# Kernel tuning notes

Hardware: AMD Instinct MI355X
Metric: run time of the kernel (lower is better)

Reference implementation:

```python
import jax, jax.numpy as jnp
import numpy as np

B, T, D = 2, 2048, 512
H, W = 8, 32
d = D // H


def setup_inputs() -> dict:
    key = jax.random.key(0)
    ks = jax.random.split(key, 9)
    s = 1.0 / np.sqrt(D)
    return {
        "x": jax.random.normal(ks[0], (B, T, D), dtype=jnp.float32),
        "wq": jax.random.normal(ks[1], (D, D), dtype=jnp.float32) * s,
        "bq": jnp.zeros((D,), dtype=jnp.float32),
        "wk": jax.random.normal(ks[2], (D, D), dtype=jnp.float32) * s,
        "bk": jnp.zeros((D,), dtype=jnp.float32),
        "wv": jax.random.normal(ks[3], (D, D), dtype=jnp.float32) * s,
        "bv": jnp.zeros((D,), dtype=jnp.float32),
        "wo": jax.random.normal(ks[4], (D, D), dtype=jnp.float32) * s,
        "bo": jnp.zeros((D,), dtype=jnp.float32),
    }


def _local_attn(x, wq, bq, wk, bk, wv, bv, wo, bo):
    Bx, Tx, Dx = x.shape
    # projections (weights stored as [D_in, D_out])
    Q = (x @ wq + bq).reshape(Bx, Tx, H, d).transpose(0, 2, 1, 3)  # [B,H,T,d]
    K = (x @ wk + bk).reshape(Bx, Tx, H, d).transpose(0, 2, 1, 3)
    V = (x @ wv + bv).reshape(Bx, Tx, H, d).transpose(0, 2, 1, 3)
    # zero-pad time axis by W on both sides (matches F.pad value=0; NO masking,
    # padded zero keys get score 0 and participate in softmax like the original)
    Kp = jnp.pad(K, ((0, 0), (0, 0), (W, W), (0, 0)))  # [B,H,T+2W,d]
    Vp = jnp.pad(V, ((0, 0), (0, 0), (W, W), (0, 0)))
    idx = jnp.arange(Tx)[:, None] + jnp.arange(2 * W + 1)[None, :]  # [T, 2W+1]
    K_loc = Kp[:, :, idx, :]  # [B,H,T,2W+1,d]
    V_loc = Vp[:, :, idx, :]
    scores = jnp.einsum("bhtd,bhtwd->bhtw", Q, K_loc) / jnp.sqrt(jnp.asarray(d, x.dtype))
    attn = jax.nn.softmax(scores, axis=-1)
    out = jnp.einsum("bhtw,bhtwd->bhtd", attn, V_loc)  # [B,H,T,d]
    out = out.transpose(0, 2, 1, 3).reshape(Bx, Tx, Dx)
    return out @ wo + bo


def reference(x, wq, bq, wk, bk, wv, bv, wo, bo):
    return _local_attn(x, wq, bq, wk, bk, wv, bv, wo, bo)
```

## Files before the change

kernel.cpp:

```cpp
#include <hip/hip_runtime.h>

using f16x8 = __attribute__((ext_vector_type(8))) _Float16;
using f16x4 = __attribute__((ext_vector_type(4))) _Float16;
using f32x4 = __attribute__((ext_vector_type(4))) float;

#define T_SEQ 2048
#define D_MODEL 512
#define NH 8
#define HD 64
#define NB 2
#define M_ROWS (NB * T_SEQ)

#define GLOAD_LDS16(g, l)                                              \
  __builtin_amdgcn_global_load_lds(                                    \
      (const __attribute__((address_space(1))) void*)(g),              \
      (__attribute__((address_space(3))) void*)(l), 16, 0, 0)

__global__ __launch_bounds__(256) void cvt_all(
    const float* __restrict__ x, const float* __restrict__ wq,
    const float* __restrict__ wk, const float* __restrict__ wv,
    const float* __restrict__ wo, const float* __restrict__ bq,
    const float* __restrict__ bk, const float* __restrict__ bv,
    _Float16* __restrict__ xh, _Float16* __restrict__ wT,
    float* __restrict__ bias3) {
  int bid = blockIdx.x;
  int i = threadIdx.x;
  if (bid < 2048) {
    int idx = (bid * 256 + i) * 4;
    float4 v = *(const float4*)(x + idx);
    f16x4 h;
    h[0] = (_Float16)v.x; h[1] = (_Float16)v.y;
    h[2] = (_Float16)v.z; h[3] = (_Float16)v.w;
    *(f16x4*)(xh + idx) = h;
    return;
  }
  bid -= 2048;
  const int z = bid >> 8;
  const int by = (bid >> 4) & 15;
  const int bx = bid & 15;
  const float* w = z == 0 ? wq : z == 1 ? wk : z == 2 ? wv : wo;
  __shared__ float t[32][33];
  int r0 = by * 32, c0 = bx * 32;
#pragma unroll
  for (int p = 0; p < 4; ++p) {
    int e = p * 256 + i;
    int row = e >> 5, col = e & 31;
    t[row][col] = w[(size_t)(r0 + row) * D_MODEL + c0 + col];
  }
  __syncthreads();
  _Float16* o = wT + (size_t)z * D_MODEL * D_MODEL;
#pragma unroll
  for (int p = 0; p < 4; ++p) {
    int e = p * 256 + i;
    int orow = e >> 5, ocol = e & 31;
    o[(size_t)(c0 + orow) * D_MODEL + r0 + ocol] = (_Float16)t[ocol][orow];
  }
  if (bx == 0 && by == 0 && z < 3) {
    const float* bb = z == 0 ? bq : z == 1 ? bk : bv;
#pragma unroll
    for (int p = 0; p < 2; ++p)
      bias3[z * D_MODEL + p * 256 + i] = bb[p * 256 + i];
  }
}

template <int OUT_F32, int BM>
__global__ __launch_bounds__(256) void gemm_bt(
    const _Float16* __restrict__ A, const _Float16* __restrict__ BtBase,
    const float* __restrict__ biasBase, void* outBase) {
  constexpr int BN = 128;
  constexpr int WROWS = (BM >= 128) ? 2 : 1;
  constexpr int WCOLS = 4 / WROWS;
  constexpr int MF = BM / WROWS / 16;
  constexpr int NF = BN / WCOLS / 16;
  constexpr int NT = D_MODEL / 32;
  const int z = blockIdx.z;
  const _Float16* Bt = BtBase + (size_t)z * D_MODEL * D_MODEL;
  const float* bias = biasBase + z * D_MODEL;
  const int m0 = blockIdx.y * BM;
  const int n0 = blockIdx.x * BN;
  __shared__ _Float16 At[2][BM * 32];
  __shared__ _Float16 Bts[2][BN * 32];
  const int tid = threadIdx.x;
  const int l = tid & 63;
  const int wv = tid >> 6;
  const int wm = wv / WCOLS, wn = wv % WCOLS;
  const int r16 = l & 15, g4 = l >> 4;
  f32x4 acc[MF][NF] = {};

  auto stage = [&](int bb, int k0) {
#pragma unroll
    for (int cc = 0; cc < BM / 64; ++cc) {
      int c = tid + cc * 256;
      int row = c >> 2, part = c & 3;
      GLOAD_LDS16(&A[(size_t)(m0 + row) * D_MODEL + k0 + part * 8],
                  &At[bb][(c - l) * 8]);
    }
#pragma unroll
    for (int cc = 0; cc < BN / 64; ++cc) {
      int c = tid + cc * 256;
      int row = c >> 2, part = c & 3;
      GLOAD_LDS16(&Bt[(size_t)(n0 + row) * D_MODEL + k0 + part * 8],
                  &Bts[bb][(c - l) * 8]);
    }
  };
  auto compute = [&](int bb) {
    f16x8 a[MF], b[NF];
#pragma unroll
    for (int mf = 0; mf < MF; ++mf)
      a[mf] = *(const f16x8*)&At[bb][(wm * (BM / WROWS) + mf * 16 + r16) * 32 +
                                     g4 * 8];
#pragma unroll
    for (int nf = 0; nf < NF; ++nf)
      b[nf] = *(const f16x8*)&Bts[bb][(wn * (BN / WCOLS) + nf * 16 + r16) * 32 +
                                      g4 * 8];
#pragma unroll
    for (int mf = 0; mf < MF; ++mf)
#pragma unroll
      for (int nf = 0; nf < NF; ++nf)
        acc[mf][nf] = __builtin_amdgcn_mfma_f32_16x16x32_f16(
            a[mf], b[nf], acc[mf][nf], 0, 0, 0);
  };

  stage(0, 0);
  __syncthreads();
#pragma unroll
  for (int t = 0; t < NT; ++t) {
    if (t + 1 < NT) stage((t + 1) & 1, (t + 1) * 32);
    compute(t & 1);
    __syncthreads();
  }

#pragma unroll
  for (int mf = 0; mf < MF; ++mf) {
#pragma unroll
    for (int nf = 0; nf < NF; ++nf) {
      int col = n0 + wn * (BN / WCOLS) + nf * 16 + r16;
      float bs = bias[col];
#pragma unroll
      for (int r = 0; r < 4; ++r) {
        int rowi = m0 + wm * (BM / WROWS) + mf * 16 + g4 * 4 + r;
        float v = acc[mf][nf][r] + bs;
        if (OUT_F32)
          ((float*)outBase)[(size_t)rowi * D_MODEL + col] = v;
        else
          ((_Float16*)outBase)[(size_t)z * M_ROWS * D_MODEL +
                               (size_t)rowi * D_MODEL + col] = (_Float16)v;
      }
    }
  }
}

__global__ __launch_bounds__(256) void local_attn(
    const _Float16* __restrict__ Q, const _Float16* __restrict__ K,
    const _Float16* __restrict__ V, _Float16* __restrict__ att) {
  const int t0 = blockIdx.x * 64;
  const int h = blockIdx.y;
  const int b = blockIdx.z;
  const int k0 = t0 - 32;
  __shared__ _Float16 Qs[64 * 64];
  __shared__ _Float16 Ks[128 * 64];
  __shared__ _Float16 Vt[64 * 136];
  __shared__ _Float16 Ps[64 * 136];
  const int tid = threadIdx.x;
  const int l = tid & 63;
  const int wv = tid >> 6;
  const size_t colbase = (size_t)h * HD;
#pragma unroll
  for (int cc = 0; cc < 2; ++cc) {
    int c = tid + cc * 256;
    int row = c >> 3, part = c & 7;
    int sp = part ^ (row & 7);
    GLOAD_LDS16(&Q[(size_t)(b * T_SEQ + t0 + row) * D_MODEL + colbase + sp * 8],
                &Qs[(c - l) * 8]);
  }
  const bool interior = (k0 >= 0) && (k0 + 128 <= T_SEQ);
  if (interior) {
#pragma unroll
    for (int cc = 0; cc < 4; ++cc) {
      int c = tid + cc * 256;
      int row = c >> 3, part = c & 7;
      int sp = part ^ (row & 7);
      GLOAD_LDS16(
          &K[(size_t)(b * T_SEQ + k0 + row) * D_MODEL + colbase + sp * 8],
          &Ks[(c - l) * 8]);
    }
  } else {
#pragma unroll
    for (int cc = 0; cc < 4; ++cc) {
      int c = tid + cc * 256;
      int row = c >> 3, part = c & 7;
      int t = k0 + row;
      f16x8 v = {};
      if (t >= 0 && t < T_SEQ)
        v = *(const f16x8*)&K[(size_t)(b * T_SEQ + t) * D_MODEL + colbase +
                              part * 8];
      *(f16x8*)&Ks[row * 64 + (part ^ (row & 7)) * 8] = v;
    }
  }
#pragma unroll
  for (int cc = 0; cc < 4; ++cc) {
    int c = tid + cc * 256;
    int row = c >> 3, part = c & 7;
    int t = k0 + row;
    f16x8 v = {};
    if (t >= 0 && t < T_SEQ)
      v = *(const f16x8*)&V[(size_t)(b * T_SEQ + t) * D_MODEL + colbase +
                            part * 8];
#pragma unroll
    for (int j = 0; j < 8; ++j) Vt[(part * 8 + j) * 136 + row] = v[j];
  }
  __syncthreads();
  const int r16 = l & 15, g4 = l >> 4;
  f32x4 s[8] = {};
#pragma unroll
  for (int kk = 0; kk < 2; ++kk) {
    int p = kk * 4 + g4;
    f16x8 a = *(const f16x8*)&Qs[(wv * 16 + r16) * 64 + (p ^ (r16 & 7)) * 8];
#pragma unroll
    for (int nf = 0; nf < 8; ++nf) {
      f16x8 bb =
          *(const f16x8*)&Ks[(nf * 16 + r16) * 64 + (p ^ (r16 & 7)) * 8];
      s[nf] = __builtin_amdgcn_mfma_f32_16x16x32_f16(a, bb, s[nf], 0, 0, 0);
    }
  }
#pragma unroll
  for (int r = 0; r < 4; ++r) {
    int ql = wv * 16 + g4 * 4 + r;
    float vals[8];
    float m = -1e30f;
#pragma unroll
    for (int nf = 0; nf < 8; ++nf) {
      int j = nf * 16 + r16;
      bool in = (j >= ql) && (j <= ql + 64);
      float sv = in ? s[nf][r] * 0.125f : -1e30f;
      vals[nf] = sv;
      m = fmaxf(m, sv);
    }
#pragma unroll
    for (int off = 1; off < 16; off <<= 1) m = fmaxf(m, __shfl_xor(m, off, 64));
    float e[8];
    float sum = 0.f;
#pragma unroll
    for (int nf = 0; nf < 8; ++nf) {
      float ev = (vals[nf] > -1e29f) ? __expf(vals[nf] - m) : 0.f;
      e[nf] = ev;
      sum += ev;
    }
#pragma unroll
    for (int off = 1; off < 16; off <<= 1) sum += __shfl_xor(sum, off, 64);
    float inv = 1.f / sum;
#pragma unroll
    for (int nf = 0; nf < 8; ++nf)
      Ps[ql * 136 + nf * 16 + r16] = (_Float16)(e[nf] * inv);
  }
  __syncthreads();
  f32x4 o[4] = {};
#pragma unroll
  for (int kk = 0; kk < 4; ++kk) {
    f16x8 a = *(const f16x8*)&Ps[(wv * 16 + r16) * 136 + kk * 32 + g4 * 8];
#pragma unroll
    for (int nf = 0; nf < 4; ++nf) {
      f16x8 bb = *(const f16x8*)&Vt[(nf * 16 + r16) * 136 + kk * 32 + g4 * 8];
      o[nf] = __builtin_amdgcn_mfma_f32_16x16x32_f16(a, bb, o[nf], 0, 0, 0);
    }
  }
#pragma unroll
  for (int nf = 0; nf < 4; ++nf)
#pragma unroll
    for (int r = 0; r < 4; ++r) {
      int row = t0 + wv * 16 + g4 * 4 + r;
      int col = nf * 16 + r16;
      att[(size_t)(b * T_SEQ + row) * D_MODEL + colbase + col] =
          (_Float16)o[nf][r];
    }
}

extern "C" void kernel_launch(void* const* d_in, const int* in_sizes, int n_in,
                              void* d_out, int out_size, void* d_ws,
                              size_t ws_size, hipStream_t stream) {
  const float* x = (const float*)d_in[0];
  const float* wq = (const float*)d_in[1];
  const float* bq = (const float*)d_in[2];
  const float* wk = (const float*)d_in[3];
  const float* bk = (const float*)d_in[4];
  const float* wv = (const float*)d_in[5];
  const float* bv = (const float*)d_in[6];
  const float* wo = (const float*)d_in[7];
  const float* bo = (const float*)d_in[8];

  char* ws = (char*)d_ws;
  _Float16* xh = (_Float16*)(ws);
  _Float16* wT = (_Float16*)(ws + (4 << 20));
  float* bias3 = (float*)(ws + (6 << 20));
  _Float16* QKV = (_Float16*)(ws + (6 << 20) + (64 << 10));
  _Float16* att = xh;

  cvt_all<<<3072, 256, 0, stream>>>(x, wq, wk, wv, wo, bq, bk, bv, xh, wT,
                                    bias3);
  gemm_bt<0, 128><<<dim3(4, 32, 3), 256, 0, stream>>>(xh, wT, bias3, QKV);
  const _Float16* Qm = QKV;
  const _Float16* Km = QKV + (size_t)M_ROWS * D_MODEL;
  const _Float16* Vm = Km + (size_t)M_ROWS * D_MODEL;
  local_attn<<<dim3(32, 8, 2), 256, 0, stream>>>(Qm, Km, Vm, att);
  gemm_bt<1, 64><<<dim3(4, 64, 1), 256, 0, stream>>>(
      att, wT + (size_t)3 * D_MODEL * D_MODEL, bo, d_out);
}
```

Before: 47.43 us.

## Fuse x fp32-to-fp16 conversion into QKV GEMM A-tile loading; load Q fragments directly

The separate x conversion pass is removed. The QKV GEMM now reads fp32 x from global memory into registers, converts it to fp16, and writes it to LDS, with the next tile's load issued before compute to keep double-buffering. Q fragments in the attention kernel are loaded straight into registers instead of through LDS. This saves a full write and re-read of x in fp16, but the QKV GEMM re-reads fp32 x once per N-block (4 times and 3 z slices) and adds register pressure and conversion work inside the main loop.

```diff
diff --git a/kernel.cpp b/kernel.cpp
--- a/kernel.cpp
+++ b/kernel.cpp
@@ -16,31 +16,17 @@
       (const __attribute__((address_space(1))) void*)(g),              \
       (__attribute__((address_space(3))) void*)(l), 16, 0, 0)
 
-__global__ __launch_bounds__(256) void cvt_all(
-    const float* __restrict__ x, const float* __restrict__ wq,
-    const float* __restrict__ wk, const float* __restrict__ wv,
-    const float* __restrict__ wo, const float* __restrict__ bq,
-    const float* __restrict__ bk, const float* __restrict__ bv,
-    _Float16* __restrict__ xh, _Float16* __restrict__ wT,
+__global__ __launch_bounds__(256) void cvt_w(
+    const float* __restrict__ wq, const float* __restrict__ wk,
+    const float* __restrict__ wv, const float* __restrict__ wo,
+    const float* __restrict__ bq, const float* __restrict__ bk,
+    const float* __restrict__ bv, _Float16* __restrict__ wT,
     float* __restrict__ bias3) {
-  int bid = blockIdx.x;
-  int i = threadIdx.x;
-  if (bid < 2048) {
-    int idx = (bid * 256 + i) * 4;
-    float4 v = *(const float4*)(x + idx);
-    f16x4 h;
-    h[0] = (_Float16)v.x; h[1] = (_Float16)v.y;
-    h[2] = (_Float16)v.z; h[3] = (_Float16)v.w;
-    *(f16x4*)(xh + idx) = h;
-    return;
-  }
-  bid -= 2048;
-  const int z = bid >> 8;
-  const int by = (bid >> 4) & 15;
-  const int bx = bid & 15;
+  const int z = blockIdx.z;
   const float* w = z == 0 ? wq : z == 1 ? wk : z == 2 ? wv : wo;
   __shared__ float t[32][33];
-  int r0 = by * 32, c0 = bx * 32;
+  int r0 = blockIdx.y * 32, c0 = blockIdx.x * 32;
+  int i = threadIdx.x;
 #pragma unroll
   for (int p = 0; p < 4; ++p) {
     int e = p * 256 + i;
@@ -55,7 +41,7 @@
     int orow = e >> 5, ocol = e & 31;
     o[(size_t)(c0 + orow) * D_MODEL + r0 + ocol] = (_Float16)t[ocol][orow];
   }
-  if (bx == 0 && by == 0 && z < 3) {
+  if (blockIdx.x == 0 && blockIdx.y == 0 && z < 3) {
     const float* bb = z == 0 ? bq : z == 1 ? bk : bv;
 #pragma unroll
     for (int p = 0; p < 2; ++p)
@@ -63,9 +49,9 @@
   }
 }
 
-template <int OUT_F32, int BM>
+template <int OUT_F32, int BM, int AF32>
 __global__ __launch_bounds__(256) void gemm_bt(
-    const _Float16* __restrict__ A, const _Float16* __restrict__ BtBase,
+    const void* __restrict__ Abase, const _Float16* __restrict__ BtBase,
     const float* __restrict__ biasBase, void* outBase) {
   constexpr int BN = 128;
   constexpr int WROWS = (BM >= 128) ? 2 : 1;
@@ -86,15 +72,44 @@
   const int wm = wv / WCOLS, wn = wv % WCOLS;
   const int r16 = l & 15, g4 = l >> 4;
   f32x4 acc[MF][NF] = {};
-
-  auto stage = [&](int bb, int k0) {
+  const float* Af = (const float*)Abase;
+  const _Float16* Ah = (const _Float16*)Abase;
+
+  float4 ar[2][2];
+
+  auto loadA = [&](int k0) {
 #pragma unroll
     for (int cc = 0; cc < BM / 64; ++cc) {
       int c = tid + cc * 256;
       int row = c >> 2, part = c & 3;
-      GLOAD_LDS16(&A[(size_t)(m0 + row) * D_MODEL + k0 + part * 8],
+      const float* src = &Af[(size_t)(m0 + row) * D_MODEL + k0 + part * 8];
+      ar[cc][0] = *(const float4*)src;
+      ar[cc][1] = *(const float4*)(src + 4);
+    }
+  };
+  auto writeA = [&](int bb) {
+#pragma unroll
+    for (int cc = 0; cc < BM / 64; ++cc) {
+      int c = tid + cc * 256;
+      f16x8 h;
+#pragma unroll
+      for (int j = 0; j < 4; ++j) {
+        h[j] = (_Float16)ar[cc][0][j];
+        h[4 + j] = (_Float16)ar[cc][1][j];
+      }
+      *(f16x8*)&At[bb][c * 8] = h;
+    }
+  };
+  auto stageA16 = [&](int bb, int k0) {
+#pragma unroll
+    for (int cc = 0; cc < BM / 64; ++cc) {
+      int c = tid + cc * 256;
+      int row = c >> 2, part = c & 3;
+      GLOAD_LDS16(&Ah[(size_t)(m0 + row) * D_MODEL + k0 + part * 8],
                   &At[bb][(c - l) * 8]);
     }
+  };
+  auto stageB = [&](int bb, int k0) {
 #pragma unroll
     for (int cc = 0; cc < BN / 64; ++cc) {
       int c = tid + cc * 256;
@@ -121,12 +136,31 @@
             a[mf], b[nf], acc[mf][nf], 0, 0, 0);
   };
 
-  stage(0, 0);
+  if constexpr (AF32) {
+    loadA(0);
+    stageB(0, 0);
+    writeA(0);
+  } else {
+    stageA16(0, 0);
+    stageB(0, 0);
+  }
   __syncthreads();
 #pragma unroll
   for (int t = 0; t < NT; ++t) {
-    if (t + 1 < NT) stage((t + 1) & 1, (t + 1) * 32);
-    compute(t & 1);
+    if constexpr (AF32) {
+      if (t + 1 < NT) {
+        loadA((t + 1) * 32);
+        stageB((t + 1) & 1, (t + 1) * 32);
+      }
+      compute(t & 1);
+      if (t + 1 < NT) writeA((t + 1) & 1);
+    } else {
+      if (t + 1 < NT) {
+        stageA16((t + 1) & 1, (t + 1) * 32);
+        stageB((t + 1) & 1, (t + 1) * 32);
+      }
+      compute(t & 1);
+    }
     __syncthreads();
   }
 
@@ -157,22 +191,19 @@
   const int h = blockIdx.y;
   const int b = blockIdx.z;
   const int k0 = t0 - 32;
-  __shared__ _Float16 Qs[64 * 64];
   __shared__ _Float16 Ks[128 * 64];
   __shared__ _Float16 Vt[64 * 136];
   __shared__ _Float16 Ps[64 * 136];
   const int tid = threadIdx.x;
   const int l = tid & 63;
   const int wv = tid >> 6;
+  const int r16 = l & 15, g4 = l >> 4;
   const size_t colbase = (size_t)h * HD;
-#pragma unroll
-  for (int cc = 0; cc < 2; ++cc) {
-    int c = tid + cc * 256;
-    int row = c >> 3, part = c & 7;
-    int sp = part ^ (row & 7);
-    GLOAD_LDS16(&Q[(size_t)(b * T_SEQ + t0 + row) * D_MODEL + colbase + sp * 8],
-                &Qs[(c - l) * 8]);
-  }
+  f16x8 qf[2];
+#pragma unroll
+  for (int kk = 0; kk < 2; ++kk)
+    qf[kk] = *(const f16x8*)&Q[(size_t)(b * T_SEQ + t0 + wv * 16 + r16) *
+                                   D_MODEL + colbase + kk * 32 + g4 * 8];
   const bool interior = (k0 >= 0) && (k0 + 128 <= T_SEQ);
   if (interior) {
 #pragma unroll
@@ -210,17 +241,15 @@
     for (int j = 0; j < 8; ++j) Vt[(part * 8 + j) * 136 + row] = v[j];
   }
   __syncthreads();
-  const int r16 = l & 15, g4 = l >> 4;
   f32x4 s[8] = {};
 #pragma unroll
   for (int kk = 0; kk < 2; ++kk) {
     int p = kk * 4 + g4;
-    f16x8 a = *(const f16x8*)&Qs[(wv * 16 + r16) * 64 + (p ^ (r16 & 7)) * 8];
 #pragma unroll
     for (int nf = 0; nf < 8; ++nf) {
       f16x8 bb =
           *(const f16x8*)&Ks[(nf * 16 + r16) * 64 + (p ^ (r16 & 7)) * 8];
-      s[nf] = __builtin_amdgcn_mfma_f32_16x16x32_f16(a, bb, s[nf], 0, 0, 0);
+      s[nf] = __builtin_amdgcn_mfma_f32_16x16x32_f16(qf[kk], bb, s[nf], 0, 0, 0);
     }
   }
 #pragma unroll
@@ -289,19 +318,18 @@
   const float* bo = (const float*)d_in[8];
 
   char* ws = (char*)d_ws;
-  _Float16* xh = (_Float16*)(ws);
-  _Float16* wT = (_Float16*)(ws + (4 << 20));
-  float* bias3 = (float*)(ws + (6 << 20));
-  _Float16* QKV = (_Float16*)(ws + (6 << 20) + (64 << 10));
-  _Float16* att = xh;
-
-  cvt_all<<<3072, 256, 0, stream>>>(x, wq, wk, wv, wo, bq, bk, bv, xh, wT,
-                                    bias3);
-  gemm_bt<0, 128><<<dim3(4, 32, 3), 256, 0, stream>>>(xh, wT, bias3, QKV);
+  _Float16* wT = (_Float16*)(ws);
+  float* bias3 = (float*)(ws + (2 << 20));
+  _Float16* QKV = (_Float16*)(ws + (4 << 20));
+  _Float16* att = (_Float16*)(ws + (16 << 20));
+
+  cvt_w<<<dim3(16, 16, 4), 256, 0, stream>>>(wq, wk, wv, wo, bq, bk, bv, wT,
+                                             bias3);
+  gemm_bt<0, 128, 1><<<dim3(4, 32, 3), 256, 0, stream>>>(x, wT, bias3, QKV);
   const _Float16* Qm = QKV;
   const _Float16* Km = QKV + (size_t)M_ROWS * D_MODEL;
   const _Float16* Vm = Km + (size_t)M_ROWS * D_MODEL;
   local_attn<<<dim3(32, 8, 2), 256, 0, stream>>>(Qm, Km, Vm, att);
-  gemm_bt<1, 64><<<dim3(4, 64, 1), 256, 0, stream>>>(
+  gemm_bt<1, 64, 0><<<dim3(4, 64, 1), 256, 0, stream>>>(
       att, wT + (size_t)3 * D_MODEL * D_MODEL, bo, d_out);
 }
```

New measurement: 48.71 us. 1.03x slower.

## Triple-buffer GEMM with swizzled LDS, load Q fragments directly in attention

Applied to the files above, without the earlier changes.

The projection GEMM moves from double to triple buffering of its LDS tiles. It waits with a vmcnt-based wait and a single barrier per k-step, so global loads run two stages ahead, and it XOR-swizzles the LDS layout to reduce bank conflicts on fragment reads. The attention kernel drops the Q shared-memory staging and loads the Q MFMA fragments straight from global memory into registers. The GEMM uses more LDS, which may lower occupancy, and the vmcnt count depends on the exact number of loads per stage.

```diff
diff --git a/kernel.cpp b/kernel.cpp
--- a/kernel.cpp
+++ b/kernel.cpp
@@ -73,13 +73,14 @@
   constexpr int MF = BM / WROWS / 16;
   constexpr int NF = BN / WCOLS / 16;
   constexpr int NT = D_MODEL / 32;
+  constexpr int LPS = BM / 64 + BN / 64;
   const int z = blockIdx.z;
   const _Float16* Bt = BtBase + (size_t)z * D_MODEL * D_MODEL;
   const float* bias = biasBase + z * D_MODEL;
   const int m0 = blockIdx.y * BM;
   const int n0 = blockIdx.x * BN;
-  __shared__ _Float16 At[2][BM * 32];
-  __shared__ _Float16 Bts[2][BN * 32];
+  __shared__ _Float16 At[3][BM * 32];
+  __shared__ _Float16 Bts[3][BN * 32];
   const int tid = threadIdx.x;
   const int l = tid & 63;
   const int wv = tid >> 6;
@@ -91,28 +92,30 @@
 #pragma unroll
     for (int cc = 0; cc < BM / 64; ++cc) {
       int c = tid + cc * 256;
-      int row = c >> 2, part = c & 3;
-      GLOAD_LDS16(&A[(size_t)(m0 + row) * D_MODEL + k0 + part * 8],
+      int row = c >> 2, sp = (c & 3) ^ (row & 3);
+      GLOAD_LDS16(&A[(size_t)(m0 + row) * D_MODEL + k0 + sp * 8],
                   &At[bb][(c - l) * 8]);
     }
 #pragma unroll
     for (int cc = 0; cc < BN / 64; ++cc) {
       int c = tid + cc * 256;
-      int row = c >> 2, part = c & 3;
-      GLOAD_LDS16(&Bt[(size_t)(n0 + row) * D_MODEL + k0 + part * 8],
+      int row = c >> 2, sp = (c & 3) ^ (row & 3);
+      GLOAD_LDS16(&Bt[(size_t)(n0 + row) * D_MODEL + k0 + sp * 8],
                   &Bts[bb][(c - l) * 8]);
     }
   };
   auto compute = [&](int bb) {
     f16x8 a[MF], b[NF];
 #pragma unroll
-    for (int mf = 0; mf < MF; ++mf)
-      a[mf] = *(const f16x8*)&At[bb][(wm * (BM / WROWS) + mf * 16 + r16) * 32 +
-                                     g4 * 8];
-#pragma unroll
-    for (int nf = 0; nf < NF; ++nf)
-      b[nf] = *(const f16x8*)&Bts[bb][(wn * (BN / WCOLS) + nf * 16 + r16) * 32 +
-                                      g4 * 8];
+    for (int mf = 0; mf < MF; ++mf) {
+      int row = wm * (BM / WROWS) + mf * 16 + r16;
+      a[mf] = *(const f16x8*)&At[bb][row * 32 + (g4 ^ (row & 3)) * 8];
+    }
+#pragma unroll
+    for (int nf = 0; nf < NF; ++nf) {
+      int row = wn * (BN / WCOLS) + nf * 16 + r16;
+      b[nf] = *(const f16x8*)&Bts[bb][row * 32 + (g4 ^ (row & 3)) * 8];
+    }
 #pragma unroll
     for (int mf = 0; mf < MF; ++mf)
 #pragma unroll
@@ -122,12 +125,16 @@
   };
 
   stage(0, 0);
-  __syncthreads();
+  stage(1, 32);
 #pragma unroll
   for (int t = 0; t < NT; ++t) {
-    if (t + 1 < NT) stage((t + 1) & 1, (t + 1) * 32);
-    compute(t & 1);
-    __syncthreads();
+    if (t + 1 < NT)
+      asm volatile("s_waitcnt vmcnt(%0)" ::"n"(LPS) : "memory");
+    else
+      asm volatile("s_waitcnt vmcnt(0)" ::: "memory");
+    __builtin_amdgcn_s_barrier();
+    compute(t % 3);
+    if (t + 2 < NT) stage((t + 2) % 3, (t + 2) * 32);
   }
 
 #pragma unroll
@@ -157,22 +164,19 @@
   const int h = blockIdx.y;
   const int b = blockIdx.z;
   const int k0 = t0 - 32;
-  __shared__ _Float16 Qs[64 * 64];
   __shared__ _Float16 Ks[128 * 64];
   __shared__ _Float16 Vt[64 * 136];
   __shared__ _Float16 Ps[64 * 136];
   const int tid = threadIdx.x;
   const int l = tid & 63;
   const int wv = tid >> 6;
+  const int r16 = l & 15, g4 = l >> 4;
   const size_t colbase = (size_t)h * HD;
-#pragma unroll
-  for (int cc = 0; cc < 2; ++cc) {
-    int c = tid + cc * 256;
-    int row = c >> 3, part = c & 7;
-    int sp = part ^ (row & 7);
-    GLOAD_LDS16(&Q[(size_t)(b * T_SEQ + t0 + row) * D_MODEL + colbase + sp * 8],
-                &Qs[(c - l) * 8]);
-  }
+  f16x8 qf[2];
+#pragma unroll
+  for (int kk = 0; kk < 2; ++kk)
+    qf[kk] = *(const f16x8*)&Q[(size_t)(b * T_SEQ + t0 + wv * 16 + r16) *
+                                   D_MODEL + colbase + kk * 32 + g4 * 8];
   const bool interior = (k0 >= 0) && (k0 + 128 <= T_SEQ);
   if (interior) {
 #pragma unroll
@@ -210,17 +214,16 @@
     for (int j = 0; j < 8; ++j) Vt[(part * 8 + j) * 136 + row] = v[j];
   }
   __syncthreads();
-  const int r16 = l & 15, g4 = l >> 4;
   f32x4 s[8] = {};
 #pragma unroll
   for (int kk = 0; kk < 2; ++kk) {
     int p = kk * 4 + g4;
-    f16x8 a = *(const f16x8*)&Qs[(wv * 16 + r16) * 64 + (p ^ (r16 & 7)) * 8];
 #pragma unroll
     for (int nf = 0; nf < 8; ++nf) {
       f16x8 bb =
           *(const f16x8*)&Ks[(nf * 16 + r16) * 64 + (p ^ (r16 & 7)) * 8];
-      s[nf] = __builtin_amdgcn_mfma_f32_16x16x32_f16(a, bb, s[nf], 0, 0, 0);
+      s[nf] =
+          __builtin_amdgcn_mfma_f32_16x16x32_f16(qf[kk], bb, s[nf], 0, 0, 0);
     }
   }
 #pragma unroll
```

Result: faster. 44.10 us (-7.0%).
